# Kernel tuning notes

Hardware: AMD Instinct MI355X
Metric: run time of the kernel (lower is better)

The kernel has to match this reference:

```python
import jax, jax.numpy as jnp
import numpy as np

N_EMBD = 1024
N_HEAD = 64

def setup_inputs() -> dict:
    key = jax.random.key(0)
    ks = jax.random.split(key, 7)
    B, T = 4, 4096
    x = jax.random.normal(ks[0], (B, T, N_EMBD), dtype=jnp.float32)
    # causal mask: True above the diagonal (masked positions)
    mask = jnp.triu(jnp.ones((T, T), dtype=bool), k=1)
    s = 1.0 / np.sqrt(N_EMBD)
    Wq = jax.random.normal(ks[1], (N_EMBD, N_HEAD), dtype=jnp.float32) * s
    bq = jnp.zeros((N_HEAD,), dtype=jnp.float32)
    Wk = jax.random.normal(ks[2], (N_EMBD, N_HEAD), dtype=jnp.float32) * s
    bk = jnp.zeros((N_HEAD,), dtype=jnp.float32)
    Wv = jax.random.normal(ks[3], (N_EMBD, N_HEAD), dtype=jnp.float32) * s
    bv = jnp.zeros((N_HEAD,), dtype=jnp.float32)
    return {"x": x, "mask": mask, "Wq": Wq, "bq": bq, "Wk": Wk, "bk": bk, "Wv": Wv, "bv": bv}

def reference(x, mask, Wq, bq, Wk, bk, Wv, bv):
    # x: [B,T,C], mask: [T,T] bool (True = masked)
    q = x @ Wq + bq            # [B,T,H]
    k = x @ Wk + bk            # [B,T,H]
    v = x @ Wv + bv            # [B,T,H]
    scale = 1.0 / jnp.sqrt(jnp.asarray(q.shape[-1], dtype=q.dtype))
    att = jnp.einsum('bth,bsh->bts', q, k) * scale   # [B,T,T]
    att = jnp.where(mask[None, :, :], -jnp.inf, att)
    att = jax.nn.softmax(att, axis=-1)
    # dropout omitted (eval mode / deterministic reference)
    return jnp.einsum('bts,bsh->bth', att, v)        # [B,T,H]
```

## Files before the change

kernel.cpp:

```cpp
#include <hip/hip_runtime.h>
#include <hip/hip_bf16.h>

#define BB 4
#define TT 4096
#define CC 1024
#define HH 64

#define QSCALE 0.18033688011112042f
#define FIXMAX2 23.083120654223414f

typedef __attribute__((ext_vector_type(8))) short short8;
typedef __attribute__((ext_vector_type(8))) ushort ushortx8;
typedef __attribute__((ext_vector_type(4))) float floatx4;

__device__ __forceinline__ ushort f2bf(float f) {
    union { float f; unsigned u; } a; a.f = f;
    const unsigned u = a.u;
    return (ushort)((u + 0x7fffu + ((u >> 16) & 1u)) >> 16);
}
__device__ __forceinline__ float bf2f(ushort h) {
    union { unsigned u; float f; } a; a.u = ((unsigned)h) << 16; return a.f;
}

__global__ __launch_bounds__(256)
void wtrans_kernel(const float* __restrict__ Wq, const float* __restrict__ Wk,
                   const float* __restrict__ Wv, ushort* __restrict__ wTf)
{
    const int tid = threadIdx.x;
    const int kc = blockIdx.x;
    #pragma unroll
    for (int it = 0; it < 6; ++it) {
        const int s = it * 256 + tid;
        const int lane = s & 63;
        const int t = s >> 6;
        const int j = t % 3;
        const int qv = t / 3;
        const int wv = qv & 3, ks = qv >> 2;
        const int r = wv * 48 + j * 16 + (lane & 15);
        const int mat = r >> 6, n = r & 63;
        const int k0 = kc * 64 + ks * 32 + (lane >> 4) * 8;
        const float* W = (mat == 0) ? Wq : (mat == 1) ? Wk : Wv;
        ushortx8 o;
        #pragma unroll
        for (int e = 0; e < 8; ++e)
            o[e] = f2bf(W[(size_t)(k0 + e) * 64 + n]);
        *(ushortx8*)(wTf + ((size_t)(kc * 24 + t) * 64 + lane) * 8) = o;
    }
}

__global__ __launch_bounds__(256)
void qkv_mfma_kernel(const float* __restrict__ x, const ushort* __restrict__ wTf,
                     const float* __restrict__ bq, const float* __restrict__ bk,
                     const float* __restrict__ bv,
                     ushort* __restrict__ q, ushort* __restrict__ k,
                     ushort* __restrict__ vT)
{
    __shared__ ushort xs[2][32 * 72];

    const int tid = threadIdx.x, w = tid >> 6, lane = tid & 63;
    const int m = lane & 15, quad = lane >> 4;
    const int row0 = blockIdx.x * 32;

    floatx4 acc[2][3];
    #pragma unroll
    for (int mi = 0; mi < 2; ++mi)
        #pragma unroll
        for (int j = 0; j < 3; ++j) acc[mi][j] = (floatx4){0.f, 0.f, 0.f, 0.f};

    const ushort* gb = wTf + (size_t)w * 1536 + lane * 8;

    const int xr = tid >> 3, xseg = tid & 7;
    const float* gx = x + (size_t)(row0 + xr) * CC + xseg * 8;

    short8 bcur[3][2], bnxt[3][2];

    #pragma unroll
    for (int j = 0; j < 3; ++j)
        #pragma unroll
        for (int ks_ = 0; ks_ < 2; ++ks_)
            bcur[j][ks_] = *(const short8*)(gb + ks_ * 6144 + j * 512);
    {
        const float4 xa = *(const float4*)(gx);
        const float4 xb = *(const float4*)(gx + 4);
        ushortx8 p;
        p[0] = f2bf(xa.x); p[1] = f2bf(xa.y); p[2] = f2bf(xa.z); p[3] = f2bf(xa.w);
        p[4] = f2bf(xb.x); p[5] = f2bf(xb.y); p[6] = f2bf(xb.z); p[7] = f2bf(xb.w);
        *(ushortx8*)(&xs[0][xr * 72 + xseg * 8]) = p;
    }
    __syncthreads();

    for (int kc = 0; kc < 16; ++kc) {
        const int cur = kc & 1;
        float4 na, nb;
        if (kc < 15) {
            const int k0n = (kc + 1) * 64;
            na = *(const float4*)(gx + k0n);
            nb = *(const float4*)(gx + k0n + 4);
            const ushort* gn = gb + (size_t)(kc + 1) * 12288;
            #pragma unroll
            for (int j = 0; j < 3; ++j)
                #pragma unroll
                for (int ks_ = 0; ks_ < 2; ++ks_)
                    bnxt[j][ks_] = *(const short8*)(gn + ks_ * 6144 + j * 512);
        }
        const ushort* xb_ = xs[cur];
        #pragma unroll
        for (int mi = 0; mi < 2; ++mi) {
            const short8 a0 = *(const short8*)(xb_ + (mi * 16 + m) * 72 + quad * 8);
            const short8 a1 = *(const short8*)(xb_ + (mi * 16 + m) * 72 + 32 + quad * 8);
            #pragma unroll
            for (int j = 0; j < 3; ++j) {
                acc[mi][j] = __builtin_amdgcn_mfma_f32_16x16x32_bf16(a0, bcur[j][0], acc[mi][j], 0, 0, 0);
                acc[mi][j] = __builtin_amdgcn_mfma_f32_16x16x32_bf16(a1, bcur[j][1], acc[mi][j], 0, 0, 0);
            }
        }
        if (kc < 15) {
            ushortx8 p;
            p[0] = f2bf(na.x); p[1] = f2bf(na.y); p[2] = f2bf(na.z); p[3] = f2bf(na.w);
            p[4] = f2bf(nb.x); p[5] = f2bf(nb.y); p[6] = f2bf(nb.z); p[7] = f2bf(nb.w);
            *(ushortx8*)(&xs[cur ^ 1][xr * 72 + xseg * 8]) = p;
            #pragma unroll
            for (int j = 0; j < 3; ++j) {
                bcur[j][0] = bnxt[j][0];
                bcur[j][1] = bnxt[j][1];
            }
        }
        __syncthreads();
    }

    const int b_ = row0 >> 12, tb = row0 & (TT - 1);
    #pragma unroll
    for (int j = 0; j < 3; ++j) {
        const int nt = w * 3 + j;
        const int mat = nt >> 2;
        const int c = (nt & 3) * 16 + m;
        const float bias = (mat == 0) ? bq[c] : (mat == 1) ? bk[c] : bv[c];
        #pragma unroll
        for (int mi = 0; mi < 2; ++mi) {
            const int gr0 = row0 + mi * 16 + quad * 4;
            if (mat == 0) {
                #pragma unroll
                for (int r = 0; r < 4; ++r)
                    q[(size_t)(gr0 + r) * HH + c] = f2bf((acc[mi][j][r] + bias) * QSCALE);
            } else if (mat == 1) {
                #pragma unroll
                for (int r = 0; r < 4; ++r)
                    k[(size_t)(gr0 + r) * HH + c] = f2bf(acc[mi][j][r] + bias);
            } else {
                ushort4 pv;
                pv.x = f2bf(acc[mi][j][0] + bias); pv.y = f2bf(acc[mi][j][1] + bias);
                pv.z = f2bf(acc[mi][j][2] + bias); pv.w = f2bf(acc[mi][j][3] + bias);
                const int t0 = tb + mi * 16 + quad * 4;
                *(ushort4*)(vT + ((size_t)b_ * HH + c) * TT + t0) = pv;
            }
        }
    }
}

__global__ __launch_bounds__(256)
void attn_mfma_kernel(const ushort* __restrict__ q, const ushort* __restrict__ k,
                      const ushort* __restrict__ vT,
                      float* __restrict__ partL, ushort* __restrict__ partO)
{
    __shared__ ushort ks[64 * 72];
    __shared__ ushort vs[64 * 72];
    __shared__ ushort ps[4][16 * 72];

    const int tid = threadIdx.x, w = tid >> 6, lane = tid & 63;
    const int m = lane & 15, quad = lane >> 4;
    const int pid = blockIdx.x;
    const int job = pid >> 3, split = pid & 7;
    const int b = job >> 6, tile = job & 63;
    const int i0 = tile * 64;
    const int nch = tile + 1;
    const int lo = (nch * split) >> 3, hi = (nch * (split + 1)) >> 3;

    const size_t qrow = ((size_t)b * TT + i0 + w * 16 + m) * HH;
    const uint4 aq0u = *(const uint4*)(q + qrow + quad * 8);
    const uint4 aq1u = *(const uint4*)(q + qrow + 32 + quad * 8);
    const short8 aq0 = *(const short8*)&aq0u;
    const short8 aq1 = *(const short8*)&aq1u;

    float lrow[4] = {0.f, 0.f, 0.f, 0.f};
    floatx4 oacc[4];
    #pragma unroll
    for (int nt = 0; nt < 4; ++nt) oacc[nt] = (floatx4){0.f, 0.f, 0.f, 0.f};

    const int iq0 = i0 + w * 16;
    for (int ch = lo; ch < hi; ++ch) {
        const int s0 = ch * 64;
        __syncthreads();
        const size_t kb = ((size_t)b * TT + s0) * HH;
        #pragma unroll
        for (int it = 0; it < 2; ++it) {
            const int t2 = it * 256 + tid;
            const int r = t2 >> 3, seg = t2 & 7;
            *(uint4*)(ks + r * 72 + seg * 8) = *(const uint4*)(k + kb + (size_t)r * HH + seg * 8);
            *(uint4*)(vs + r * 72 + seg * 8) = *(const uint4*)(vT + ((size_t)b * HH + r) * TT + s0 + seg * 8);
        }
        __syncthreads();

        floatx4 sc[4];
        #pragma unroll
        for (int nt = 0; nt < 4; ++nt) {
            const short8 b0 = *(const short8*)(ks + (nt * 16 + m) * 72 + quad * 8);
            const short8 b1 = *(const short8*)(ks + (nt * 16 + m) * 72 + 32 + quad * 8);
            floatx4 s_ = (floatx4){0.f, 0.f, 0.f, 0.f};
            s_ = __builtin_amdgcn_mfma_f32_16x16x32_bf16(aq0, b0, s_, 0, 0, 0);
            s_ = __builtin_amdgcn_mfma_f32_16x16x32_bf16(aq1, b1, s_, 0, 0, 0);
            sc[nt] = s_;
        }

        const bool need_mask = (s0 + 63 > iq0);
        #pragma unroll
        for (int r = 0; r < 4; ++r) {
            float t0 = sc[0][r] - FIXMAX2;
            float t1 = sc[1][r] - FIXMAX2;
            float t2 = sc[2][r] - FIXMAX2;
            float t3 = sc[3][r] - FIXMAX2;
            if (need_mask) {
                const int dlim = iq0 + quad * 4 + r - s0 - m;
                if (0  > dlim) t0 = -1e30f;
                if (16 > dlim) t1 = -1e30f;
                if (32 > dlim) t2 = -1e30f;
                if (48 > dlim) t3 = -1e30f;
            }
            const float p0 = __builtin_amdgcn_exp2f(t0);
            const float p1 = __builtin_amdgcn_exp2f(t1);
            const float p2 = __builtin_amdgcn_exp2f(t2);
            const float p3 = __builtin_amdgcn_exp2f(t3);
            lrow[r] += (p0 + p1) + (p2 + p3);
            ushort* pr = ps[w] + (quad * 4 + r) * 72;
            pr[m]      = f2bf(p0);
            pr[16 + m] = f2bf(p1);
            pr[32 + m] = f2bf(p2);
            pr[48 + m] = f2bf(p3);
        }

        #pragma unroll
        for (int ks_ = 0; ks_ < 2; ++ks_) {
            const short8 ap = *(const short8*)(ps[w] + m * 72 + ks_ * 32 + quad * 8);
            #pragma unroll
            for (int nt = 0; nt < 4; ++nt) {
                const short8 bv_ = *(const short8*)(vs + (nt * 16 + m) * 72 + ks_ * 32 + quad * 8);
                oacc[nt] = __builtin_amdgcn_mfma_f32_16x16x32_bf16(ap, bv_, oacc[nt], 0, 0, 0);
            }
        }
    }

    #pragma unroll
    for (int r = 0; r < 4; ++r) {
        float s = lrow[r];
        s += __shfl_xor(s, 1); s += __shfl_xor(s, 2);
        s += __shfl_xor(s, 4); s += __shfl_xor(s, 8);
        lrow[r] = s;
    }
    if (m == 0) {
        #pragma unroll
        for (int r = 0; r < 4; ++r)
            partL[(size_t)pid * 64 + w * 16 + quad * 4 + r] = lrow[r];
    }
    ushort* po = partO + ((size_t)pid * 64 + w * 16) * 64;
    #pragma unroll
    for (int r = 0; r < 4; ++r) {
        const int row = quad * 4 + r;
        #pragma unroll
        for (int nt = 0; nt < 4; ++nt)
            po[row * 64 + nt * 16 + m] = f2bf(oacc[nt][r]);
    }
}

__global__ __launch_bounds__(256)
void attn_combine_kernel(const float* __restrict__ partL,
                         const ushort* __restrict__ partO, float* __restrict__ out)
{
    const int job = blockIdx.x;
    const int tid = threadIdx.x;
    const int row = tid >> 2, dq = tid & 3;

    float L = 0.f;
    #pragma unroll
    for (int s = 0; s < 8; ++s) L += partL[(size_t)(job * 8 + s) * 64 + row];
    const float inv = 1.f / L;

    float o[16];
    #pragma unroll
    for (int i = 0; i < 16; ++i) o[i] = 0.f;
    #pragma unroll
    for (int s = 0; s < 8; ++s) {
        const ushort* po = partO + (((size_t)(job * 8 + s) * 64 + row) * 64 + dq * 16);
        #pragma unroll
        for (int i2 = 0; i2 < 2; ++i2) {
            const ushort4 pa = *(const ushort4*)(po + i2 * 8);
            const ushort4 pb = *(const ushort4*)(po + i2 * 8 + 4);
            o[i2*8+0] += bf2f(pa.x); o[i2*8+1] += bf2f(pa.y);
            o[i2*8+2] += bf2f(pa.z); o[i2*8+3] += bf2f(pa.w);
            o[i2*8+4] += bf2f(pb.x); o[i2*8+5] += bf2f(pb.y);
            o[i2*8+6] += bf2f(pb.z); o[i2*8+7] += bf2f(pb.w);
        }
    }
    float4* dst = (float4*)(out + ((size_t)job * 64 + row) * 64 + dq * 16);
    #pragma unroll
    for (int i = 0; i < 4; ++i) {
        float4 v; v.x = o[i*4]*inv; v.y = o[i*4+1]*inv; v.z = o[i*4+2]*inv; v.w = o[i*4+3]*inv;
        dst[i] = v;
    }
}

extern "C" void kernel_launch(void* const* d_in, const int* in_sizes, int n_in,
                              void* d_out, int out_size, void* d_ws, size_t ws_size,
                              hipStream_t stream) {
    (void)in_sizes; (void)n_in; (void)out_size; (void)ws_size;
    const float* x  = (const float*)d_in[0];
    const float* Wq = (const float*)d_in[2];
    const float* bq = (const float*)d_in[3];
    const float* Wk = (const float*)d_in[4];
    const float* bk = (const float*)d_in[5];
    const float* Wv = (const float*)d_in[6];
    const float* bv = (const float*)d_in[7];
    float* out = (float*)d_out;

    char* ws = (char*)d_ws;
    ushort* wTf   = (ushort*)ws;
    ushort* qb    = (ushort*)(ws + 393216);
    ushort* kb    = qb + (size_t)BB * TT * HH;
    ushort* vTb   = kb + (size_t)BB * TT * HH;
    float*  partL = (float*) (ws + 6684672);
    ushort* partO = (ushort*)(ws + 7208960);

    wtrans_kernel   <<<16, 256, 0, stream>>>(Wq, Wk, Wv, wTf);
    qkv_mfma_kernel <<<(BB * TT) / 32, 256, 0, stream>>>(x, wTf, bq, bk, bv, qb, kb, vTb);
    attn_mfma_kernel<<<BB * 64 * 8, 256, 0, stream>>>(qb, kb, vTb, partL, partO);
    attn_combine_kernel<<<BB * 64, 256, 0, stream>>>(partL, partO, out);
}
```

Measured before the change: 196.4 us.

## Load x directly into MFMA registers in QKV projection, drop LDS staging

The QKV projection kernel no longer stages x through shared memory with barriers. Each lane loads its own fp32 x fragment from global memory, packs it to bf16 with the hardware packed-convert instruction, and feeds it straight to MFMA. The K loop is software-pipelined two steps deep in registers. Blocks now cover 16 rows instead of 32, doubling the grid, which removes syncs and LDS traffic but makes each of the four waves reload the same x rows, raising redundant global/L2 reads.

```diff
diff --git a/kernel.cpp b/kernel.cpp
--- a/kernel.cpp
+++ b/kernel.cpp
@@ -20,6 +20,19 @@
 }
 __device__ __forceinline__ float bf2f(ushort h) {
     union { unsigned u; float f; } a; a.u = ((unsigned)h) << 16; return a.f;
+}
+__device__ __forceinline__ unsigned cvtpk(float a, float b) {
+    unsigned r;
+    asm("v_cvt_pk_bf16_f32 %0, %1, %2" : "=v"(r) : "v"(a), "v"(b));
+    return r;
+}
+__device__ __forceinline__ short8 pack8(float4 a, float4 b) {
+    union { unsigned u[4]; short8 s; } r;
+    r.u[0] = cvtpk(a.x, a.y);
+    r.u[1] = cvtpk(a.z, a.w);
+    r.u[2] = cvtpk(b.x, b.y);
+    r.u[3] = cvtpk(b.z, b.w);
+    return r.s;
 }
 
 __global__ __launch_bounds__(256)
@@ -55,104 +68,76 @@
                      ushort* __restrict__ q, ushort* __restrict__ k,
                      ushort* __restrict__ vT)
 {
-    __shared__ ushort xs[2][32 * 72];
-
     const int tid = threadIdx.x, w = tid >> 6, lane = tid & 63;
     const int m = lane & 15, quad = lane >> 4;
-    const int row0 = blockIdx.x * 32;
-
-    floatx4 acc[2][3];
-    #pragma unroll
-    for (int mi = 0; mi < 2; ++mi)
-        #pragma unroll
-        for (int j = 0; j < 3; ++j) acc[mi][j] = (floatx4){0.f, 0.f, 0.f, 0.f};
+    const int row0 = blockIdx.x * 16;
+
+    floatx4 acc[3];
+    #pragma unroll
+    for (int j = 0; j < 3; ++j) acc[j] = (floatx4){0.f, 0.f, 0.f, 0.f};
 
     const ushort* gb = wTf + (size_t)w * 1536 + lane * 8;
-
-    const int xr = tid >> 3, xseg = tid & 7;
-    const float* gx = x + (size_t)(row0 + xr) * CC + xseg * 8;
-
-    short8 bcur[3][2], bnxt[3][2];
-
-    #pragma unroll
-    for (int j = 0; j < 3; ++j)
-        #pragma unroll
-        for (int ks_ = 0; ks_ < 2; ++ks_)
-            bcur[j][ks_] = *(const short8*)(gb + ks_ * 6144 + j * 512);
-    {
-        const float4 xa = *(const float4*)(gx);
-        const float4 xb = *(const float4*)(gx + 4);
-        ushortx8 p;
-        p[0] = f2bf(xa.x); p[1] = f2bf(xa.y); p[2] = f2bf(xa.z); p[3] = f2bf(xa.w);
-        p[4] = f2bf(xb.x); p[5] = f2bf(xb.y); p[6] = f2bf(xb.z); p[7] = f2bf(xb.w);
-        *(ushortx8*)(&xs[0][xr * 72 + xseg * 8]) = p;
-    }
-    __syncthreads();
-
-    for (int kc = 0; kc < 16; ++kc) {
-        const int cur = kc & 1;
-        float4 na, nb;
-        if (kc < 15) {
-            const int k0n = (kc + 1) * 64;
-            na = *(const float4*)(gx + k0n);
-            nb = *(const float4*)(gx + k0n + 4);
-            const ushort* gn = gb + (size_t)(kc + 1) * 12288;
-            #pragma unroll
-            for (int j = 0; j < 3; ++j)
-                #pragma unroll
-                for (int ks_ = 0; ks_ < 2; ++ks_)
-                    bnxt[j][ks_] = *(const short8*)(gn + ks_ * 6144 + j * 512);
-        }
-        const ushort* xb_ = xs[cur];
-        #pragma unroll
-        for (int mi = 0; mi < 2; ++mi) {
-            const short8 a0 = *(const short8*)(xb_ + (mi * 16 + m) * 72 + quad * 8);
-            const short8 a1 = *(const short8*)(xb_ + (mi * 16 + m) * 72 + 32 + quad * 8);
-            #pragma unroll
-            for (int j = 0; j < 3; ++j) {
-                acc[mi][j] = __builtin_amdgcn_mfma_f32_16x16x32_bf16(a0, bcur[j][0], acc[mi][j], 0, 0, 0);
-                acc[mi][j] = __builtin_amdgcn_mfma_f32_16x16x32_bf16(a1, bcur[j][1], acc[mi][j], 0, 0, 0);
-            }
-        }
-        if (kc < 15) {
-            ushortx8 p;
-            p[0] = f2bf(na.x); p[1] = f2bf(na.y); p[2] = f2bf(na.z); p[3] = f2bf(na.w);
-            p[4] = f2bf(nb.x); p[5] = f2bf(nb.y); p[6] = f2bf(nb.z); p[7] = f2bf(nb.w);
-            *(ushortx8*)(&xs[cur ^ 1][xr * 72 + xseg * 8]) = p;
-            #pragma unroll
-            for (int j = 0; j < 3; ++j) {
-                bcur[j][0] = bnxt[j][0];
-                bcur[j][1] = bnxt[j][1];
-            }
-        }
-        __syncthreads();
-    }
-
-    const int b_ = row0 >> 12, tb = row0 & (TT - 1);
+    const float* gx = x + (size_t)(row0 + m) * CC + quad * 8;
+
+#define LDX(kc, A0, A1, A2, A3) { const float* g_ = gx + (kc) * 64;           \
+        A0 = *(const float4*)(g_);      A1 = *(const float4*)(g_ + 4);        \
+        A2 = *(const float4*)(g_ + 32); A3 = *(const float4*)(g_ + 36); }
+#define LDB(kc, B00, B01, B10, B11, B20, B21) {                               \
+        const ushort* g_ = gb + (size_t)(kc) * 12288;                         \
+        B00 = *(const short8*)(g_);        B01 = *(const short8*)(g_ + 6144); \
+        B10 = *(const short8*)(g_ + 512);  B11 = *(const short8*)(g_ + 6656); \
+        B20 = *(const short8*)(g_ + 1024); B21 = *(const short8*)(g_ + 7168); }
+#define STEP(A0, A1, A2, A3, B00, B01, B10, B11, B20, B21) {                  \
+        const short8 a0 = pack8(A0, A1), a1 = pack8(A2, A3);                  \
+        acc[0] = __builtin_amdgcn_mfma_f32_16x16x32_bf16(a0, B00, acc[0], 0, 0, 0); \
+        acc[0] = __builtin_amdgcn_mfma_f32_16x16x32_bf16(a1, B01, acc[0], 0, 0, 0); \
+        acc[1] = __builtin_amdgcn_mfma_f32_16x16x32_bf16(a0, B10, acc[1], 0, 0, 0); \
+        acc[1] = __builtin_amdgcn_mfma_f32_16x16x32_bf16(a1, B11, acc[1], 0, 0, 0); \
+        acc[2] = __builtin_amdgcn_mfma_f32_16x16x32_bf16(a0, B20, acc[2], 0, 0, 0); \
+        acc[2] = __builtin_amdgcn_mfma_f32_16x16x32_bf16(a1, B21, acc[2], 0, 0, 0); }
+
+    float4 pa0, pa1, pa2, pa3, qa0, qa1, qa2, qa3;
+    short8 pb0, pb1, pb2, pb3, pb4, pb5;
+    short8 qb0, qb1, qb2, qb3, qb4, qb5;
+
+    LDX(0, pa0, pa1, pa2, pa3);
+    LDB(0, pb0, pb1, pb2, pb3, pb4, pb5);
+    #pragma unroll
+    for (int kc = 0; kc < 16; kc += 2) {
+        LDX(kc + 1, qa0, qa1, qa2, qa3);
+        LDB(kc + 1, qb0, qb1, qb2, qb3, qb4, qb5);
+        STEP(pa0, pa1, pa2, pa3, pb0, pb1, pb2, pb3, pb4, pb5);
+        if (kc < 14) {
+            LDX(kc + 2, pa0, pa1, pa2, pa3);
+            LDB(kc + 2, pb0, pb1, pb2, pb3, pb4, pb5);
+        }
+        STEP(qa0, qa1, qa2, qa3, qb0, qb1, qb2, qb3, qb4, qb5);
+    }
+#undef LDX
+#undef LDB
+#undef STEP
+
+    const int gr0 = row0 + quad * 4;
+    const int b_ = gr0 >> 12, t0 = gr0 & (TT - 1);
     #pragma unroll
     for (int j = 0; j < 3; ++j) {
         const int nt = w * 3 + j;
         const int mat = nt >> 2;
         const int c = (nt & 3) * 16 + m;
         const float bias = (mat == 0) ? bq[c] : (mat == 1) ? bk[c] : bv[c];
-        #pragma unroll
-        for (int mi = 0; mi < 2; ++mi) {
-            const int gr0 = row0 + mi * 16 + quad * 4;
-            if (mat == 0) {
-                #pragma unroll
-                for (int r = 0; r < 4; ++r)
-                    q[(size_t)(gr0 + r) * HH + c] = f2bf((acc[mi][j][r] + bias) * QSCALE);
-            } else if (mat == 1) {
-                #pragma unroll
-                for (int r = 0; r < 4; ++r)
-                    k[(size_t)(gr0 + r) * HH + c] = f2bf(acc[mi][j][r] + bias);
-            } else {
-                ushort4 pv;
-                pv.x = f2bf(acc[mi][j][0] + bias); pv.y = f2bf(acc[mi][j][1] + bias);
-                pv.z = f2bf(acc[mi][j][2] + bias); pv.w = f2bf(acc[mi][j][3] + bias);
-                const int t0 = tb + mi * 16 + quad * 4;
-                *(ushort4*)(vT + ((size_t)b_ * HH + c) * TT + t0) = pv;
-            }
+        if (mat == 0) {
+            #pragma unroll
+            for (int r = 0; r < 4; ++r)
+                q[(size_t)(gr0 + r) * HH + c] = f2bf((acc[j][r] + bias) * QSCALE);
+        } else if (mat == 1) {
+            #pragma unroll
+            for (int r = 0; r < 4; ++r)
+                k[(size_t)(gr0 + r) * HH + c] = f2bf(acc[j][r] + bias);
+        } else {
+            ushort4 pv;
+            pv.x = f2bf(acc[j][0] + bias); pv.y = f2bf(acc[j][1] + bias);
+            pv.z = f2bf(acc[j][2] + bias); pv.w = f2bf(acc[j][3] + bias);
+            *(ushort4*)(vT + ((size_t)b_ * HH + c) * TT + t0) = pv;
         }
     }
 }
@@ -329,7 +314,7 @@
     ushort* partO = (ushort*)(ws + 7208960);
 
     wtrans_kernel   <<<16, 256, 0, stream>>>(Wq, Wk, Wv, wTf);
-    qkv_mfma_kernel <<<(BB * TT) / 32, 256, 0, stream>>>(x, wTf, bq, bk, bv, qb, kb, vTb);
+    qkv_mfma_kernel <<<(BB * TT) / 16, 256, 0, stream>>>(x, wTf, bq, bk, bv, qb, kb, vTb);
     attn_mfma_kernel<<<BB * 64 * 8, 256, 0, stream>>>(qb, kb, vTb, partL, partO);
     attn_combine_kernel<<<BB * 64, 256, 0, stream>>>(partL, partO, out);
 }
```

Result: slower. 218.9 us (+11.4%).

## Prefetch next K/V chunk into registers and raise wave priority around MFMA

Applied to the files above, without the earlier changes.

The attention loop now loads the next K and V^T chunk from global memory into registers while the current chunk is being computed, then writes them to LDS at the start of the next iteration. This hides global-load latency behind the QK^T, softmax and PV work instead of stalling after each barrier. It also wraps the two MFMA sections with s_setprio so waves issuing matrix instructions get scheduling priority. The cost is extra registers per thread for the prefetch buffers, which may lower occupancy.

```diff
diff --git a/kernel.cpp b/kernel.cpp
--- a/kernel.cpp
+++ b/kernel.cpp
@@ -186,21 +186,44 @@
     #pragma unroll
     for (int nt = 0; nt < 4; ++nt) oacc[nt] = (floatx4){0.f, 0.f, 0.f, 0.f};
 
+    const int trow = tid >> 3, tseg = tid & 7;
+
+    uint4 nk[2], nv[2];
+    if (lo < hi) {
+        const int s0 = lo * 64;
+        const size_t kb = ((size_t)b * TT + s0) * HH;
+        #pragma unroll
+        for (int it = 0; it < 2; ++it) {
+            const int r = it * 32 + trow;
+            nk[it] = *(const uint4*)(k + kb + (size_t)r * HH + tseg * 8);
+            nv[it] = *(const uint4*)(vT + ((size_t)b * HH + r) * TT + s0 + tseg * 8);
+        }
+    }
+
     const int iq0 = i0 + w * 16;
     for (int ch = lo; ch < hi; ++ch) {
+        __syncthreads();
+        #pragma unroll
+        for (int it = 0; it < 2; ++it) {
+            const int r = it * 32 + trow;
+            *(uint4*)(ks + r * 72 + tseg * 8) = nk[it];
+            *(uint4*)(vs + r * 72 + tseg * 8) = nv[it];
+        }
+        if (ch + 1 < hi) {
+            const int s0n = (ch + 1) * 64;
+            const size_t kbn = ((size_t)b * TT + s0n) * HH;
+            #pragma unroll
+            for (int it = 0; it < 2; ++it) {
+                const int r = it * 32 + trow;
+                nk[it] = *(const uint4*)(k + kbn + (size_t)r * HH + tseg * 8);
+                nv[it] = *(const uint4*)(vT + ((size_t)b * HH + r) * TT + s0n + tseg * 8);
+            }
+        }
+        __syncthreads();
+
         const int s0 = ch * 64;
-        __syncthreads();
-        const size_t kb = ((size_t)b * TT + s0) * HH;
-        #pragma unroll
-        for (int it = 0; it < 2; ++it) {
-            const int t2 = it * 256 + tid;
-            const int r = t2 >> 3, seg = t2 & 7;
-            *(uint4*)(ks + r * 72 + seg * 8) = *(const uint4*)(k + kb + (size_t)r * HH + seg * 8);
-            *(uint4*)(vs + r * 72 + seg * 8) = *(const uint4*)(vT + ((size_t)b * HH + r) * TT + s0 + seg * 8);
-        }
-        __syncthreads();
-
         floatx4 sc[4];
+        __builtin_amdgcn_s_setprio(1);
         #pragma unroll
         for (int nt = 0; nt < 4; ++nt) {
             const short8 b0 = *(const short8*)(ks + (nt * 16 + m) * 72 + quad * 8);
@@ -210,6 +233,7 @@
             s_ = __builtin_amdgcn_mfma_f32_16x16x32_bf16(aq1, b1, s_, 0, 0, 0);
             sc[nt] = s_;
         }
+        __builtin_amdgcn_s_setprio(0);
 
         const bool need_mask = (s0 + 63 > iq0);
         #pragma unroll
@@ -237,6 +261,7 @@
             pr[48 + m] = f2bf(p3);
         }
 
+        __builtin_amdgcn_s_setprio(1);
         #pragma unroll
         for (int ks_ = 0; ks_ < 2; ++ks_) {
             const short8 ap = *(const short8*)(ps[w] + m * 72 + ks_ * 32 + quad * 8);
@@ -246,6 +271,7 @@
                 oacc[nt] = __builtin_amdgcn_mfma_f32_16x16x32_bf16(ap, bv_, oacc[nt], 0, 0, 0);
             }
         }
+        __builtin_amdgcn_s_setprio(0);
     }
 
     #pragma unroll
```

Measured after the change: 221.3 us. 12.7% more time.

## Load K/V MFMA fragments directly from global memory, drop shared staging and barriers

Applied to the files above, without the earlier changes.

The attention kernel stops staging each 64-row K and V^T chunk through shared memory. Each wave now loads its MFMA B-operand fragments straight from global memory into registers, which removes the two __syncthreads per chunk and the LDS round trip. It also adds s_setprio around the MFMA sections and a launch_bounds occupancy hint of 2. The cost is that all four waves redundantly fetch the same K/V data through L1/L2, and the fragment registers raise register pressure.

```diff
diff --git a/kernel.cpp b/kernel.cpp
--- a/kernel.cpp
+++ b/kernel.cpp
@@ -157,13 +157,11 @@
     }
 }
 
-__global__ __launch_bounds__(256)
+__global__ __launch_bounds__(256, 2)
 void attn_mfma_kernel(const ushort* __restrict__ q, const ushort* __restrict__ k,
                       const ushort* __restrict__ vT,
                       float* __restrict__ partL, ushort* __restrict__ partO)
 {
-    __shared__ ushort ks[64 * 72];
-    __shared__ ushort vs[64 * 72];
     __shared__ ushort ps[4][16 * 72];
 
     const int tid = threadIdx.x, w = tid >> 6, lane = tid & 63;
@@ -186,30 +184,38 @@
     #pragma unroll
     for (int nt = 0; nt < 4; ++nt) oacc[nt] = (floatx4){0.f, 0.f, 0.f, 0.f};
 
+    const ushort* kfb = k  + ((size_t)b * TT + m) * HH + quad * 8;
+    const ushort* vfb = vT + ((size_t)b * HH + m) * TT + quad * 8;
+
     const int iq0 = i0 + w * 16;
     for (int ch = lo; ch < hi; ++ch) {
         const int s0 = ch * 64;
-        __syncthreads();
-        const size_t kb = ((size_t)b * TT + s0) * HH;
-        #pragma unroll
-        for (int it = 0; it < 2; ++it) {
-            const int t2 = it * 256 + tid;
-            const int r = t2 >> 3, seg = t2 & 7;
-            *(uint4*)(ks + r * 72 + seg * 8) = *(const uint4*)(k + kb + (size_t)r * HH + seg * 8);
-            *(uint4*)(vs + r * 72 + seg * 8) = *(const uint4*)(vT + ((size_t)b * HH + r) * TT + s0 + seg * 8);
-        }
-        __syncthreads();
+
+        short8 vf[4][2];
+        #pragma unroll
+        for (int nt = 0; nt < 4; ++nt) {
+            const ushort* vp = vfb + (size_t)(nt * 16) * TT + s0;
+            vf[nt][0] = *(const short8*)(vp);
+            vf[nt][1] = *(const short8*)(vp + 32);
+        }
+        short8 kf[4][2];
+        #pragma unroll
+        for (int nt = 0; nt < 4; ++nt) {
+            const ushort* kp = kfb + (size_t)(s0 + nt * 16) * HH;
+            kf[nt][0] = *(const short8*)(kp);
+            kf[nt][1] = *(const short8*)(kp + 32);
+        }
 
         floatx4 sc[4];
+        __builtin_amdgcn_s_setprio(1);
         #pragma unroll
         for (int nt = 0; nt < 4; ++nt) {
-            const short8 b0 = *(const short8*)(ks + (nt * 16 + m) * 72 + quad * 8);
-            const short8 b1 = *(const short8*)(ks + (nt * 16 + m) * 72 + 32 + quad * 8);
             floatx4 s_ = (floatx4){0.f, 0.f, 0.f, 0.f};
-            s_ = __builtin_amdgcn_mfma_f32_16x16x32_bf16(aq0, b0, s_, 0, 0, 0);
-            s_ = __builtin_amdgcn_mfma_f32_16x16x32_bf16(aq1, b1, s_, 0, 0, 0);
+            s_ = __builtin_amdgcn_mfma_f32_16x16x32_bf16(aq0, kf[nt][0], s_, 0, 0, 0);
+            s_ = __builtin_amdgcn_mfma_f32_16x16x32_bf16(aq1, kf[nt][1], s_, 0, 0, 0);
             sc[nt] = s_;
         }
+        __builtin_amdgcn_s_setprio(0);
 
         const bool need_mask = (s0 + 63 > iq0);
         #pragma unroll
@@ -237,15 +243,15 @@
             pr[48 + m] = f2bf(p3);
         }
 
+        __builtin_amdgcn_s_setprio(1);
         #pragma unroll
         for (int ks_ = 0; ks_ < 2; ++ks_) {
             const short8 ap = *(const short8*)(ps[w] + m * 72 + ks_ * 32 + quad * 8);
             #pragma unroll
-            for (int nt = 0; nt < 4; ++nt) {
-                const short8 bv_ = *(const short8*)(vs + (nt * 16 + m) * 72 + ks_ * 32 + quad * 8);
-                oacc[nt] = __builtin_amdgcn_mfma_f32_16x16x32_bf16(ap, bv_, oacc[nt], 0, 0, 0);
-            }
-        }
+            for (int nt = 0; nt < 4; ++nt)
+                oacc[nt] = __builtin_amdgcn_mfma_f32_16x16x32_bf16(ap, vf[nt][ks_], oacc[nt], 0, 0, 0);
+        }
+        __builtin_amdgcn_s_setprio(0);
     }
 
     #pragma unroll
```

Measured after the change: 250.7 us. 1.28x slower.
